# Performance work log

Measured on AMD Instinct MI355X. Metric: run time of the kernel, lower is better.

Reference implementation:

```python
import jax, jax.numpy as jnp
import numpy as np

B, S, E, H, DH = 4, 2048, 1024, 16, 64  # batch, seq, embed, heads, head_dim


def setup_inputs() -> dict:
    key = jax.random.key(0)
    k0, k1, k2, k3 = jax.random.split(key, 4)
    scale = 1.0 / np.sqrt(E).astype(np.float32)
    embedded = jax.random.normal(k0, (B, S, E), jnp.float32)
    Wq = jax.random.normal(k1, (H, E, DH), jnp.float32) * scale
    Wk = jax.random.normal(k2, (H, E, DH), jnp.float32) * scale
    Wv = jax.random.normal(k3, (H, E, DH), jnp.float32) * scale
    return {"embedded": embedded, "Wq": Wq, "Wk": Wk, "Wv": Wv}


def reference(embedded, Wq, Wk, Wv):
    # Batched QKV projections across all heads (replaces per-head nn.Linear loop)
    q = jnp.einsum('bse,hed->bhsd', embedded, Wq)
    k = jnp.einsum('bse,hed->bhsd', embedded, Wk)
    v = jnp.einsum('bse,hed->bhsd', embedded, Wv)
    head_dim = q.shape[-1]
    scores = jnp.einsum('bhqd,bhkd->bhqk', q, k) / jnp.sqrt(jnp.asarray(head_dim, q.dtype))
    seq = scores.shape[-1]
    causal = jnp.tril(jnp.ones((seq, seq), dtype=bool))  # lower-triangular causal mask
    scores = jnp.where(causal, scores, jnp.finfo(scores.dtype).min)
    attn = jax.nn.softmax(scores, axis=-1)
    out = jnp.einsum('bhqk,bhkd->bhqd', attn, v)
    # concatenate heads along the feature dim (torch.cat(..., dim=2))
    b, h, s, d = out.shape
    return out.transpose(0, 2, 1, 3).reshape(b, s, h * d)
```

## Files before the change

kernel.cpp:

```cpp
#include <hip/hip_runtime.h>


typedef short bf16x4 __attribute__((ext_vector_type(4)));
typedef short bf16x8 __attribute__((ext_vector_type(8)));
typedef float f32x4 __attribute__((ext_vector_type(4)));
typedef unsigned short u16x4 __attribute__((ext_vector_type(4)));
typedef unsigned short u16x8 __attribute__((ext_vector_type(8)));

#define SCL 0.1803368801111204f

static __device__ __forceinline__ unsigned short f2bf(float f) {
  unsigned int u = __builtin_bit_cast(unsigned int, f);
  u += 0x7fffu + ((u >> 16) & 1u);
  return (unsigned short)(u >> 16);
}

static __device__ __forceinline__ void gload16(const void* g, void* l) {
  __builtin_amdgcn_global_load_lds((__attribute__((address_space(1))) void*)g,
                                   (__attribute__((address_space(3))) void*)l, 16, 0, 0);
}

__global__ __launch_bounds__(256) void convs(const float* __restrict__ x,
                                             const float* __restrict__ Wq,
                                             const float* __restrict__ Wk,
                                             const float* __restrict__ Wv,
                                             unsigned short* __restrict__ Xb,
                                             unsigned short* __restrict__ Wt) {
  const int bid = blockIdx.x;
  const int t = threadIdx.x;
  if (bid < 768) {
    __shared__ __align__(16) unsigned short tile[64][72];
    const int p = bid >> 8, he = bid & 255;
    const float* Wsrc = (p == 0) ? Wq : ((p == 1) ? Wk : Wv);
    const int h = he >> 4, et = he & 15;
    const float* src = Wsrc + (h * 1024 + et * 64) * 64;
#pragma unroll
    for (int i = 0; i < 4; ++i) {
      int c = i * 256 + t;
      int r = c >> 4, cc = (c & 15) * 4;
      float4 v = *(const float4*)(src + r * 64 + cc);
      tile[r][cc + 0] = f2bf(v.x); tile[r][cc + 1] = f2bf(v.y);
      tile[r][cc + 2] = f2bf(v.z); tile[r][cc + 3] = f2bf(v.w);
    }
    __syncthreads();
#pragma unroll
    for (int i = 0; i < 2; ++i) {
      int c = i * 256 + t;
      int d = c >> 3, ec = (c & 7) * 8;
      u16x8 o;
#pragma unroll
      for (int j = 0; j < 8; ++j) o[j] = tile[ec + j][d];
      *(u16x8*)(Wt + (p * 1024 + h * 64 + d) * 1024 + et * 64 + ec) = o;
    }
  } else {
    const int n4 = 2097152;
    int i0 = (bid - 768) * 256 + t;
    const int stride = 2048 * 256;
    for (int c = i0; c < n4; c += stride) {
      float4 v = ((const float4*)x)[c];
      u16x4 o;
      o[0] = f2bf(v.x); o[1] = f2bf(v.y); o[2] = f2bf(v.z); o[3] = f2bf(v.w);
      ((u16x4*)Xb)[c] = o;
    }
  }
}

__global__ __launch_bounds__(512, 2) void qkv_gemm(const unsigned short* __restrict__ Xb,
                                                   const unsigned short* __restrict__ Wt,
                                                   unsigned short* __restrict__ Qb,
                                                   unsigned short* __restrict__ Kb,
                                                   unsigned short* __restrict__ Vtb) {
  __shared__ __align__(16) unsigned short L[3][2][256 * 32];

  const int t = threadIdx.x, lane = t & 63, w = t >> 6;
  const int wr = w >> 2, wc = w & 3, c16 = lane & 15, g = lane >> 4;

  const int bid = blockIdx.x;
  const int xcd = bid & 7, l = bid >> 3;
  const int nt = l >> 2;
  const int m0 = (xcd * 4 + (l & 3)) * 256;
  const int p = nt >> 2;
  const int nb0 = (nt & 3) * 256;

  f32x4 acc[8][4] = {};

  const int srow = t >> 2;
  const int scl = (t & 3) ^ ((srow & 3) ^ ((srow >> 2) & 3));
  const int chp = (g ^ ((c16 & 3) ^ ((c16 >> 2) & 3))) * 8;

#define STAGE(KT, AB, HALF, BUF)                                                   \
  {                                                                                \
    const unsigned short* s_ =                                                     \
        (((AB) == 0) ? (Xb + (m0 + (HALF)*128) * 1024)                             \
                     : (Wt + (p * 1024 + nb0 + (HALF)*128) * 1024)) +              \
        (KT)*32 + srow * 1024 + scl * 8;                                           \
    gload16(s_, &L[BUF][AB][(HALF)*4096 + w * 512]);                               \
  }
#define LDA(BUF, MI) (*(const bf16x8*)&L[BUF][0][(wr * 128 + (MI)*16 + c16) * 32 + chp])
#define LDB(BUF, NI) (*(const bf16x8*)&L[BUF][1][(wc * 64 + (NI)*16 + c16) * 32 + chp])

  STAGE(0, 0, 0, 0); STAGE(0, 0, 1, 0); STAGE(0, 1, 0, 0); STAGE(0, 1, 1, 0);
  STAGE(1, 0, 0, 1); STAGE(1, 0, 1, 1); STAGE(1, 1, 0, 1); STAGE(1, 1, 1, 1);

  int buf = 0;
#pragma unroll 1
  for (int kt = 0; kt < 32; ++kt) {
    const int sbuf = (buf == 0) ? 2 : buf - 1;
    if (kt < 31) { asm volatile("s_waitcnt vmcnt(4)" ::: "memory"); }
    else         { asm volatile("s_waitcnt vmcnt(0)" ::: "memory"); }
    __builtin_amdgcn_s_barrier();

    bf16x8 bq[4], aq[4];
#pragma unroll
    for (int ni = 0; ni < 4; ++ni) bq[ni] = LDB(buf, ni);
#pragma unroll
    for (int mi = 0; mi < 4; ++mi) aq[mi] = LDA(buf, mi);
    if (kt < 30) { STAGE(kt + 2, 0, 0, sbuf); STAGE(kt + 2, 0, 1, sbuf); }
    __builtin_amdgcn_s_setprio(1);
    if (p != 2) {
#pragma unroll
      for (int q = 0; q < 4; ++q)
#pragma unroll
        for (int ni = 0; ni < 4; ++ni)
          acc[q][ni] = __builtin_amdgcn_mfma_f32_16x16x32_bf16(aq[q], bq[ni], acc[q][ni], 0, 0, 0);
    } else {
#pragma unroll
      for (int q = 0; q < 4; ++q)
#pragma unroll
        for (int ni = 0; ni < 4; ++ni)
          acc[q][ni] = __builtin_amdgcn_mfma_f32_16x16x32_bf16(bq[ni], aq[q], acc[q][ni], 0, 0, 0);
    }
    __builtin_amdgcn_s_setprio(0);

    bf16x8 aq2[4];
#pragma unroll
    for (int mi = 0; mi < 4; ++mi) aq2[mi] = LDA(buf, 4 + mi);
    if (kt < 30) { STAGE(kt + 2, 1, 0, sbuf); STAGE(kt + 2, 1, 1, sbuf); }
    __builtin_amdgcn_s_setprio(1);
    if (p != 2) {
#pragma unroll
      for (int q = 0; q < 4; ++q)
#pragma unroll
        for (int ni = 0; ni < 4; ++ni)
          acc[4 + q][ni] = __builtin_amdgcn_mfma_f32_16x16x32_bf16(aq2[q], bq[ni], acc[4 + q][ni], 0, 0, 0);
    } else {
#pragma unroll
      for (int q = 0; q < 4; ++q)
#pragma unroll
        for (int ni = 0; ni < 4; ++ni)
          acc[4 + q][ni] = __builtin_amdgcn_mfma_f32_16x16x32_bf16(bq[ni], aq2[q], acc[4 + q][ni], 0, 0, 0);
    }
    __builtin_amdgcn_s_setprio(0);

    buf = (buf == 2) ? 0 : buf + 1;
  }

  if (p != 2) {
    unsigned short* dst = (p == 0) ? Qb : Kb;
#pragma unroll
    for (int mi = 0; mi < 8; ++mi)
#pragma unroll
      for (int ni = 0; ni < 4; ++ni)
#pragma unroll
        for (int r = 0; r < 4; ++r) {
          int m_g = m0 + wr * 128 + mi * 16 + g * 4 + r;
          int n_g = nb0 + wc * 64 + ni * 16 + c16;
          int b = m_g >> 11, s = m_g & 2047;
          dst[((b * 16 + (n_g >> 6)) * 2048 + s) * 64 + (n_g & 63)] = f2bf(acc[mi][ni][r]);
        }
  } else {
#pragma unroll
    for (int mi = 0; mi < 8; ++mi)
#pragma unroll
      for (int ni = 0; ni < 4; ++ni)
#pragma unroll
        for (int r = 0; r < 4; ++r) {
          int n_g = nb0 + wc * 64 + ni * 16 + g * 4 + r;
          int m_g = m0 + wr * 128 + mi * 16 + c16;
          int b = m_g >> 11, s = m_g & 2047;
          int sp = (s & ~31) | ((s << 1) & 24) | ((s >> 2) & 4) | (s & 3);
          Vtb[((b * 16 + (n_g >> 6)) * 64 + (n_g & 63)) * 2048 + sp] = f2bf(acc[mi][ni][r]);
        }
  }
#undef STAGE
#undef LDA
#undef LDB
}

__global__ __launch_bounds__(256) void attn(const unsigned short* __restrict__ Qb,
                                            const unsigned short* __restrict__ Kb,
                                            const unsigned short* __restrict__ Vtb,
                                            float* __restrict__ out) {
  const int bid = blockIdx.x;
  const int xcd = bid & 7, slot = bid >> 3;
  const int bh = xcd * 8 + (slot >> 3);
  const int pp = slot & 7;
  const int b = bh >> 4, h = bh & 15;
  const int t = threadIdx.x, lane = t & 63, w = t >> 6;
  const int g = lane >> 4, c = lane & 15;

  __shared__ __align__(16) unsigned short Ks[2][64][72];
  __shared__ __align__(16) unsigned short Vs[2][64][72];

  for (int job = 0; job < 2; ++job) {
    const int qt = job ? pp : 15 - pp;
    const int q0 = qt * 128;
    const int ktiles = 2 * qt + 2;

    bf16x8 qf[2][2];
#pragma unroll
    for (int mi = 0; mi < 2; ++mi)
#pragma unroll
      for (int kc = 0; kc < 2; ++kc)
        qf[mi][kc] = *(const bf16x8*)(Qb + ((bh * 2048 + q0 + w * 32 + mi * 16 + c) << 6)
                                         + kc * 32 + g * 8);

    f32x4 o_acc[2][4] = {};
    float m_r[2] = {-INFINITY, -INFINITY};
    float l_r[2] = {0.f, 0.f};

    uint4 kr[2], vr[2];
#pragma unroll
    for (int i = 0; i < 2; ++i) {
      int cid = i * 256 + t;
      kr[i] = *(const uint4*)(Kb + ((bh * 2048) << 6) + cid * 8);
      vr[i] = *(const uint4*)(Vtb + ((bh * 64 + (cid >> 3)) << 11) + (cid & 7) * 8);
    }
#pragma unroll
    for (int i = 0; i < 2; ++i) {
      int cid = i * 256 + t;
      *(uint4*)&Ks[0][cid >> 3][(cid & 7) * 8] = kr[i];
      *(uint4*)&Vs[0][cid >> 3][(cid & 7) * 8] = vr[i];
    }
    __syncthreads();

    for (int kt = 0; kt < ktiles; ++kt) {
      const int cur = kt & 1;
      if (kt + 1 < ktiles) {
        const int kv0n = (kt + 1) * 64;
#pragma unroll
        for (int i = 0; i < 2; ++i) {
          int cid = i * 256 + t;
          kr[i] = *(const uint4*)(Kb + ((bh * 2048 + kv0n) << 6) + cid * 8);
          vr[i] = *(const uint4*)(Vtb + ((bh * 64 + (cid >> 3)) << 11) + kv0n + (cid & 7) * 8);
        }
      }

      f32x4 sc[2][4];
#pragma unroll
      for (int sub = 0; sub < 4; ++sub) {
        bf16x8 kf0 = *(const bf16x8*)&Ks[cur][sub * 16 + c][g * 8];
        bf16x8 kf1 = *(const bf16x8*)&Ks[cur][sub * 16 + c][32 + g * 8];
#pragma unroll
        for (int mi = 0; mi < 2; ++mi) {
          f32x4 z = {};
          z = __builtin_amdgcn_mfma_f32_16x16x32_bf16(kf0, qf[mi][0], z, 0, 0, 0);
          z = __builtin_amdgcn_mfma_f32_16x16x32_bf16(kf1, qf[mi][1], z, 0, 0, 0);
          sc[mi][sub] = z;
        }
      }

      if (kt >= 2 * qt) {
        const int koff = (kt - 2 * qt) * 64;
#pragma unroll
        for (int mi = 0; mi < 2; ++mi) {
          const int q_l = w * 32 + mi * 16 + c;
#pragma unroll
          for (int sub = 0; sub < 4; ++sub)
#pragma unroll
            for (int r = 0; r < 4; ++r)
              if (koff + sub * 16 + 4 * g + r > q_l) sc[mi][sub][r] = -INFINITY;
        }
      }

      float mx[2];
#pragma unroll
      for (int mi = 0; mi < 2; ++mi) {
        float v0 = fmaxf(fmaxf(sc[mi][0][0], sc[mi][0][1]), fmaxf(sc[mi][0][2], sc[mi][0][3]));
        float v1 = fmaxf(fmaxf(sc[mi][1][0], sc[mi][1][1]), fmaxf(sc[mi][1][2], sc[mi][1][3]));
        float v2 = fmaxf(fmaxf(sc[mi][2][0], sc[mi][2][1]), fmaxf(sc[mi][2][2], sc[mi][2][3]));
        float v3 = fmaxf(fmaxf(sc[mi][3][0], sc[mi][3][1]), fmaxf(sc[mi][3][2], sc[mi][3][3]));
        float v = fmaxf(fmaxf(v0, v1), fmaxf(v2, v3));
        v = fmaxf(v, __shfl_xor(v, 16));
        v = fmaxf(v, __shfl_xor(v, 32));
        mx[mi] = v;
      }

      bool need = (mx[0] > m_r[0] + 44.f) || (mx[1] > m_r[1] + 44.f);
      if (__any(need)) {
#pragma unroll
        for (int mi = 0; mi < 2; ++mi) {
          float mnew = fmaxf(m_r[mi], mx[mi]);
          float corr = __builtin_amdgcn_exp2f((m_r[mi] - mnew) * SCL);
          m_r[mi] = mnew;
          l_r[mi] *= corr;
#pragma unroll
          for (int ni = 0; ni < 4; ++ni) o_acc[mi][ni] *= corr;
        }
      }

      bf16x8 pb[2][2];
#pragma unroll
      for (int mi = 0; mi < 2; ++mi) {
        const float a = -m_r[mi] * SCL;
        float s = 0.f;
#pragma unroll
        for (int sub = 0; sub < 4; ++sub)
#pragma unroll
          for (int r = 0; r < 4; ++r) {
            float e = __builtin_amdgcn_exp2f(fmaf(sc[mi][sub][r], SCL, a));
            sc[mi][sub][r] = e;
            s += e;
          }
        s += __shfl_xor(s, 16);
        s += __shfl_xor(s, 32);
        l_r[mi] += s;
        unsigned int* p32l = (unsigned int*)&pb[mi][0];
        unsigned int* p32h = (unsigned int*)&pb[mi][1];
#pragma unroll
        for (int jj = 0; jj < 4; ++jj) {
          const int sub = jj >> 1, r0 = (jj & 1) * 2;
          unsigned int lo_, hi_;
          asm("v_cvt_pk_bf16_f32 %0, %1, %2"
              : "=v"(lo_) : "v"(sc[mi][sub][r0]), "v"(sc[mi][sub][r0 + 1]));
          asm("v_cvt_pk_bf16_f32 %0, %1, %2"
              : "=v"(hi_) : "v"(sc[mi][2 + sub][r0]), "v"(sc[mi][2 + sub][r0 + 1]));
          p32l[jj] = lo_;
          p32h[jj] = hi_;
        }
      }

#pragma unroll
      for (int ni = 0; ni < 4; ++ni)
#pragma unroll
        for (int half = 0; half < 2; ++half) {
          bf16x8 vt = *(const bf16x8*)&Vs[cur][ni * 16 + c][half * 32 + g * 8];
#pragma unroll
          for (int mi = 0; mi < 2; ++mi)
            o_acc[mi][ni] = __builtin_amdgcn_mfma_f32_16x16x32_bf16(vt, pb[mi][half],
                                                                    o_acc[mi][ni], 0, 0, 0);
        }

      if (kt + 1 < ktiles) {
#pragma unroll
        for (int i = 0; i < 2; ++i) {
          int cid = i * 256 + t;
          *(uint4*)&Ks[cur ^ 1][cid >> 3][(cid & 7) * 8] = kr[i];
          *(uint4*)&Vs[cur ^ 1][cid >> 3][(cid & 7) * 8] = vr[i];
        }
      }
      __syncthreads();
    }

#pragma unroll
    for (int mi = 0; mi < 2; ++mi) {
      const float inv = 1.f / l_r[mi];
      const int q_g = q0 + w * 32 + mi * 16 + c;
      float* orow = out + (b * 2048 + q_g) * 1024 + h * 64;
#pragma unroll
      for (int ni = 0; ni < 4; ++ni) {
        f32x4 o = o_acc[mi][ni] * inv;
        *(f32x4*)(orow + ni * 16 + 4 * g) = o;
      }
    }
  }
}

extern "C" void kernel_launch(void* const* d_in, const int* in_sizes, int n_in,
                              void* d_out, int out_size, void* d_ws, size_t ws_size,
                              hipStream_t stream) {
  const float* emb = (const float*)d_in[0];
  const float* Wq  = (const float*)d_in[1];
  const float* Wk  = (const float*)d_in[2];
  const float* Wv  = (const float*)d_in[3];
  char* ws = (char*)d_ws;
  unsigned short* Xb  = (unsigned short*)(ws + 0);
  unsigned short* Wt  = (unsigned short*)(ws + 16777216);
  unsigned short* Qb  = (unsigned short*)(ws + 23068672);
  unsigned short* Kb  = (unsigned short*)(ws + 39845888);
  unsigned short* Vtb = (unsigned short*)(ws + 56623104);
  float* out = (float*)d_out;

  convs<<<2816, 256, 0, stream>>>(emb, Wq, Wk, Wv, Xb, Wt);
  qkv_gemm<<<384, 512, 0, stream>>>(Xb, Wt, Qb, Kb, Vtb);
  attn<<<512, 256, 0, stream>>>(Qb, Kb, Vtb, out);
}
```

Baseline: 166.8 us.

## Fuse both query-tile jobs into one KV sweep sharing loaded K/V tiles

The attention kernel previously ran its two query tiles (15-pp and pp) one after the other, streaming K/V tiles from global memory twice. Now both tiles' Q fragments and accumulators stay live and a single pass over the longer tile's KV range serves both, with the shorter tile processed only while kt is within its own range. This removes redundant K/V global loads, LDS stores and barriers for the overlapping tiles. In exchange it roughly doubles the live accumulator and Q registers, which may lower occupancy or cause spills.

```diff
diff --git a/kernel.cpp b/kernel.cpp
--- a/kernel.cpp
+++ b/kernel.cpp
@@ -202,50 +202,54 @@
   __shared__ __align__(16) unsigned short Ks[2][64][72];
   __shared__ __align__(16) unsigned short Vs[2][64][72];
 
-  for (int job = 0; job < 2; ++job) {
-    const int qt = job ? pp : 15 - pp;
-    const int q0 = qt * 128;
-    const int ktiles = 2 * qt + 2;
-
-    bf16x8 qf[2][2];
-#pragma unroll
-    for (int mi = 0; mi < 2; ++mi)
-#pragma unroll
-      for (int kc = 0; kc < 2; ++kc)
-        qf[mi][kc] = *(const bf16x8*)(Qb + ((bh * 2048 + q0 + w * 32 + mi * 16 + c) << 6)
-                                         + kc * 32 + g * 8);
-
-    f32x4 o_acc[2][4] = {};
-    float m_r[2] = {-INFINITY, -INFINITY};
-    float l_r[2] = {0.f, 0.f};
-
-    uint4 kr[2], vr[2];
-#pragma unroll
-    for (int i = 0; i < 2; ++i) {
-      int cid = i * 256 + t;
-      kr[i] = *(const uint4*)(Kb + ((bh * 2048) << 6) + cid * 8);
-      vr[i] = *(const uint4*)(Vtb + ((bh * 64 + (cid >> 3)) << 11) + (cid & 7) * 8);
-    }
-#pragma unroll
-    for (int i = 0; i < 2; ++i) {
-      int cid = i * 256 + t;
-      *(uint4*)&Ks[0][cid >> 3][(cid & 7) * 8] = kr[i];
-      *(uint4*)&Vs[0][cid >> 3][(cid & 7) * 8] = vr[i];
-    }
-    __syncthreads();
-
-    for (int kt = 0; kt < ktiles; ++kt) {
-      const int cur = kt & 1;
-      if (kt + 1 < ktiles) {
-        const int kv0n = (kt + 1) * 64;
-#pragma unroll
-        for (int i = 0; i < 2; ++i) {
-          int cid = i * 256 + t;
-          kr[i] = *(const uint4*)(Kb + ((bh * 2048 + kv0n) << 6) + cid * 8);
-          vr[i] = *(const uint4*)(Vtb + ((bh * 64 + (cid >> 3)) << 11) + kv0n + (cid & 7) * 8);
-        }
-      }
-
+  const int qt0 = 15 - pp, qt1 = pp;
+  const int q00 = qt0 * 128, q01 = qt1 * 128;
+  const int ktiles0 = 2 * qt0 + 2, ktiles1 = 2 * qt1 + 2;
+
+  bf16x8 qf0[2][2], qf1[2][2];
+#pragma unroll
+  for (int mi = 0; mi < 2; ++mi)
+#pragma unroll
+    for (int kc = 0; kc < 2; ++kc) {
+      qf0[mi][kc] = *(const bf16x8*)(Qb + ((bh * 2048 + q00 + w * 32 + mi * 16 + c) << 6)
+                                        + kc * 32 + g * 8);
+      qf1[mi][kc] = *(const bf16x8*)(Qb + ((bh * 2048 + q01 + w * 32 + mi * 16 + c) << 6)
+                                        + kc * 32 + g * 8);
+    }
+
+  f32x4 oa0[2][4] = {}, oa1[2][4] = {};
+  float m0v[2] = {-INFINITY, -INFINITY}, l0v[2] = {0.f, 0.f};
+  float m1v[2] = {-INFINITY, -INFINITY}, l1v[2] = {0.f, 0.f};
+
+  uint4 kr[2], vr[2];
+#pragma unroll
+  for (int i = 0; i < 2; ++i) {
+    int cid = i * 256 + t;
+    kr[i] = *(const uint4*)(Kb + ((bh * 2048) << 6) + cid * 8);
+    vr[i] = *(const uint4*)(Vtb + ((bh * 64 + (cid >> 3)) << 11) + (cid & 7) * 8);
+  }
+#pragma unroll
+  for (int i = 0; i < 2; ++i) {
+    int cid = i * 256 + t;
+    *(uint4*)&Ks[0][cid >> 3][(cid & 7) * 8] = kr[i];
+    *(uint4*)&Vs[0][cid >> 3][(cid & 7) * 8] = vr[i];
+  }
+  __syncthreads();
+
+  for (int kt = 0; kt < ktiles0; ++kt) {
+    const int cur = kt & 1;
+    if (kt + 1 < ktiles0) {
+      const int kv0n = (kt + 1) * 64;
+#pragma unroll
+      for (int i = 0; i < 2; ++i) {
+        int cid = i * 256 + t;
+        kr[i] = *(const uint4*)(Kb + ((bh * 2048 + kv0n) << 6) + cid * 8);
+        vr[i] = *(const uint4*)(Vtb + ((bh * 64 + (cid >> 3)) << 11) + kv0n + (cid & 7) * 8);
+      }
+    }
+
+    auto process = [&](f32x4(&oacc)[2][4], float(&mr)[2], float(&lr)[2],
+                       bf16x8(&qf)[2][2], int qtj) {
       f32x4 sc[2][4];
 #pragma unroll
       for (int sub = 0; sub < 4; ++sub) {
@@ -260,8 +264,8 @@
         }
       }
 
-      if (kt >= 2 * qt) {
-        const int koff = (kt - 2 * qt) * 64;
+      if (kt >= 2 * qtj) {
+        const int koff = (kt - 2 * qtj) * 64;
 #pragma unroll
         for (int mi = 0; mi < 2; ++mi) {
           const int q_l = w * 32 + mi * 16 + c;
@@ -286,23 +290,23 @@
         mx[mi] = v;
       }
 
-      bool need = (mx[0] > m_r[0] + 44.f) || (mx[1] > m_r[1] + 44.f);
+      bool need = (mx[0] > mr[0] + 44.f) || (mx[1] > mr[1] + 44.f);
       if (__any(need)) {
 #pragma unroll
         for (int mi = 0; mi < 2; ++mi) {
-          float mnew = fmaxf(m_r[mi], mx[mi]);
-          float corr = __builtin_amdgcn_exp2f((m_r[mi] - mnew) * SCL);
-          m_r[mi] = mnew;
-          l_r[mi] *= corr;
-#pragma unroll
-          for (int ni = 0; ni < 4; ++ni) o_acc[mi][ni] *= corr;
+          float mnew = fmaxf(mr[mi], mx[mi]);
+          float corr = __builtin_amdgcn_exp2f((mr[mi] - mnew) * SCL);
+          mr[mi] = mnew;
+          lr[mi] *= corr;
+#pragma unroll
+          for (int ni = 0; ni < 4; ++ni) oacc[mi][ni] *= corr;
         }
       }
 
       bf16x8 pb[2][2];
 #pragma unroll
       for (int mi = 0; mi < 2; ++mi) {
-        const float a = -m_r[mi] * SCL;
+        const float a = -mr[mi] * SCL;
         float s = 0.f;
 #pragma unroll
         for (int sub = 0; sub < 4; ++sub)
@@ -314,7 +318,7 @@
           }
         s += __shfl_xor(s, 16);
         s += __shfl_xor(s, 32);
-        l_r[mi] += s;
+        lr[mi] += s;
         unsigned int* p32l = (unsigned int*)&pb[mi][0];
         unsigned int* p32h = (unsigned int*)&pb[mi][1];
 #pragma unroll
@@ -337,31 +341,39 @@
           bf16x8 vt = *(const bf16x8*)&Vs[cur][ni * 16 + c][half * 32 + g * 8];
 #pragma unroll
           for (int mi = 0; mi < 2; ++mi)
-            o_acc[mi][ni] = __builtin_amdgcn_mfma_f32_16x16x32_bf16(vt, pb[mi][half],
-                                                                    o_acc[mi][ni], 0, 0, 0);
-        }
-
-      if (kt + 1 < ktiles) {
-#pragma unroll
-        for (int i = 0; i < 2; ++i) {
-          int cid = i * 256 + t;
-          *(uint4*)&Ks[cur ^ 1][cid >> 3][(cid & 7) * 8] = kr[i];
-          *(uint4*)&Vs[cur ^ 1][cid >> 3][(cid & 7) * 8] = vr[i];
-        }
-      }
-      __syncthreads();
-    }
-
-#pragma unroll
-    for (int mi = 0; mi < 2; ++mi) {
-      const float inv = 1.f / l_r[mi];
-      const int q_g = q0 + w * 32 + mi * 16 + c;
-      float* orow = out + (b * 2048 + q_g) * 1024 + h * 64;
-#pragma unroll
-      for (int ni = 0; ni < 4; ++ni) {
-        f32x4 o = o_acc[mi][ni] * inv;
-        *(f32x4*)(orow + ni * 16 + 4 * g) = o;
-      }
+            oacc[mi][ni] = __builtin_amdgcn_mfma_f32_16x16x32_bf16(vt, pb[mi][half],
+                                                                   oacc[mi][ni], 0, 0, 0);
+        }
+    };
+
+    process(oa0, m0v, l0v, qf0, qt0);
+    if (kt < ktiles1) process(oa1, m1v, l1v, qf1, qt1);
+
+    if (kt + 1 < ktiles0) {
+#pragma unroll
+      for (int i = 0; i < 2; ++i) {
+        int cid = i * 256 + t;
+        *(uint4*)&Ks[cur ^ 1][cid >> 3][(cid & 7) * 8] = kr[i];
+        *(uint4*)&Vs[cur ^ 1][cid >> 3][(cid & 7) * 8] = vr[i];
+      }
+    }
+    __syncthreads();
+  }
+
+#pragma unroll
+  for (int mi = 0; mi < 2; ++mi) {
+    const float inv0 = 1.f / l0v[mi];
+    const float inv1 = 1.f / l1v[mi];
+    const int qg0 = q00 + w * 32 + mi * 16 + c;
+    const int qg1 = q01 + w * 32 + mi * 16 + c;
+    float* orow0 = out + (b * 2048 + qg0) * 1024 + h * 64;
+    float* orow1 = out + (b * 2048 + qg1) * 1024 + h * 64;
+#pragma unroll
+    for (int ni = 0; ni < 4; ++ni) {
+      f32x4 o0 = oa0[mi][ni] * inv0;
+      f32x4 o1 = oa1[mi][ni] * inv1;
+      *(f32x4*)(orow0 + ni * 16 + 4 * g) = o0;
+      *(f32x4*)(orow1 + ni * 16 + 4 * g) = o1;
     }
   }
 }
```

Result: slower. 192.7 us (+15.6%).
